# Performance work log

Measured on AMD Instinct MI355X. Metric: run time of the kernel, lower is better.

## Reference

```python
import jax, jax.numpy as jnp
import numpy as np

B, S, E, H, EDGE = 2, 2048, 512, 8, 16
D = E // H  # head_dim = 64


def setup_inputs() -> dict:
    key = jax.random.key(0)
    ks = jax.random.split(key, 10)
    s = 0.02
    return {
        "q": jax.random.normal(ks[0], (B, S, E), dtype=jnp.float32),
        "k": jax.random.normal(ks[1], (B, S, E), dtype=jnp.float32),
        "v": jax.random.normal(ks[2], (B, S, E), dtype=jnp.float32),
        "p": jax.random.normal(ks[3], (B, S, S, EDGE), dtype=jnp.float32),
        "in_proj_w": jax.random.normal(ks[4], (3 * E, E), dtype=jnp.float32) * s,
        "in_proj_b": jnp.zeros((3 * E,), dtype=jnp.float32),
        "out_proj_w": jax.random.normal(ks[5], (E, E), dtype=jnp.float32) * s,
        "out_proj_b": jnp.zeros((E,), dtype=jnp.float32),
        "edge_w": jax.random.normal(ks[6], (H, EDGE), dtype=jnp.float32) * s,
        "edge_b": jnp.zeros((H,), dtype=jnp.float32),
    }


def reference(q, k, v, p, in_proj_w, in_proj_b, out_proj_w, out_proj_b, edge_w, edge_b):
    b, s, e = q.shape
    # edge features -> per-head additive bias: [b,sq,sk,edge] -> [b,h,sq,sk]
    bias = jnp.einsum("bqke,he->bhqk", p, edge_w) + edge_b[None, :, None, None]

    # packed qkv projections (torch Linear: y = x W^T + b)
    wq, wk, wv = jnp.split(in_proj_w, 3, axis=0)
    bq, bk, bv = jnp.split(in_proj_b, 3, axis=0)
    qh = (q @ wq.T + bq).reshape(b, s, H, D).transpose(0, 2, 1, 3)  # bhqd
    kh = (k @ wk.T + bk).reshape(b, s, H, D).transpose(0, 2, 1, 3)  # bhkd
    vh = (v @ wv.T + bv).reshape(b, s, H, D).transpose(0, 2, 1, 3)  # bhkd

    scale = 1.0 / jnp.sqrt(jnp.float32(D))
    scores = jnp.einsum("bhqd,bhkd->bhqk", qh, kh) * scale + bias
    attn = jax.nn.softmax(scores, axis=-1)
    ctx = jnp.einsum("bhqk,bhkd->bhqd", attn, vh)  # [b,h,s,d]
    ctx = ctx.transpose(0, 2, 1, 3).reshape(b, s, e)
    return ctx @ out_proj_w.T + out_proj_b
```

## Files before the change

kernel.cpp:

```cpp
#include <hip/hip_runtime.h>

#define NB 2
#define NS 2048
#define NE 512
#define NH 8
#define ND 64
#define NEDGE 16

typedef unsigned short u16;
typedef __attribute__((ext_vector_type(4))) float f32x4;
typedef __attribute__((ext_vector_type(8))) short bf16x8;

__device__ __forceinline__ u16 f2bf(float f) {
  unsigned u = __float_as_uint(f);
  u += 0x7FFFu + ((u >> 16) & 1u);
  return (u16)(u >> 16);
}
__device__ __forceinline__ float bf2f(u16 h) {
  return __uint_as_float(((unsigned)h) << 16);
}
__device__ __forceinline__ void gload16(const void* g, void* l) {
  __builtin_amdgcn_global_load_lds(
      (const __attribute__((address_space(1))) unsigned*)g,
      (__attribute__((address_space(3))) unsigned*)l, 16, 0, 0);
}

__global__ void k_cvt(const float* __restrict__ in, u16* __restrict__ out, int n4) {
  int i = blockIdx.x * 256 + threadIdx.x;
  if (i >= n4) return;
  float4 v = ((const float4*)in)[i];
  ushort4 o;
  o.x = f2bf(v.x); o.y = f2bf(v.y); o.z = f2bf(v.z); o.w = f2bf(v.w);
  ((ushort4*)out)[i] = o;
}

__device__ __forceinline__ void gemm128_core(const u16* __restrict__ A,
                                             const u16* __restrict__ W,
                                             u16* As, u16* Bs,
                                             int mt, f32x4 acc[4][4]) {
  const int tid = threadIdx.x, wave = tid >> 6, lane = tid & 63;
  const int g = lane >> 4, c = lane & 15;
  const int wm = wave >> 1, wn = wave & 1;
  for (int kt = 0; kt < 16; ++kt) {
#pragma unroll
    for (int r = 0; r < 2; ++r) {
      int seg = wave + 4 * r;
      int idx = seg * 64 + lane;
      int row = idx >> 2, colB = idx & 3;
      gload16(A + (size_t)(mt * 128 + row) * 512 + kt * 32 + colB * 8,
              (char*)As + seg * 1024);
      gload16(W + (size_t)row * 512 + kt * 32 + colB * 8,
              (char*)Bs + seg * 1024);
    }
    __syncthreads();
    bf16x8 af[4], bw[4];
#pragma unroll
    for (int mb = 0; mb < 4; ++mb)
      af[mb] = *(const bf16x8*)&As[(wm * 64 + mb * 16 + c) * 32 + 8 * g];
#pragma unroll
    for (int nb = 0; nb < 4; ++nb)
      bw[nb] = *(const bf16x8*)&Bs[(wn * 64 + nb * 16 + c) * 32 + 8 * g];
#pragma unroll
    for (int mb = 0; mb < 4; ++mb)
#pragma unroll
      for (int nb = 0; nb < 4; ++nb)
        acc[mb][nb] = __builtin_amdgcn_mfma_f32_16x16x32_bf16(
            af[mb], bw[nb], acc[mb][nb], 0, 0, 0);
    __syncthreads();
  }
}

__launch_bounds__(256)
__global__ void k_proj(const u16* __restrict__ qbf, const u16* __restrict__ kbf,
                       const u16* __restrict__ vbf, const u16* __restrict__ wbf,
                       const float* __restrict__ bin,
                       u16* __restrict__ qh, u16* __restrict__ kh,
                       u16* __restrict__ vt) {
  __shared__ __align__(16) u16 As[4096];
  __shared__ __align__(16) u16 Bs[4096];
  const int tid = threadIdx.x, wave = tid >> 6, lane = tid & 63;
  const int g = lane >> 4, c = lane & 15;
  const int wm = wave >> 1, wn = wave & 1;
  const int mt = blockIdx.x;
  const int chunk = blockIdx.y >> 2, ntl = blockIdx.y & 3;
  const u16* A = chunk == 0 ? qbf : (chunk == 1 ? kbf : vbf);
  const u16* W = wbf + (size_t)(chunk * 512 + ntl * 128) * 512;

  f32x4 acc[4][4];
#pragma unroll
  for (int i = 0; i < 4; ++i)
#pragma unroll
    for (int j = 0; j < 4; ++j) acc[i][j] = (f32x4){0.f, 0.f, 0.f, 0.f};

  gemm128_core(A, W, As, Bs, mt, acc);

#pragma unroll
  for (int mb = 0; mb < 4; ++mb) {
#pragma unroll
    for (int nb = 0; nb < 4; ++nb) {
      int ncl = ntl * 128 + wn * 64 + nb * 16 + c;
      float bv = bin[chunk * 512 + ncl];
      int h = ncl >> 6, d = ncl & 63;
      int m0 = mt * 128 + wm * 64 + mb * 16 + g * 4;
      int b = m0 >> 11, s0 = m0 & 2047;
      if (chunk == 2) {
        ushort4 o;
        o.x = f2bf(acc[mb][nb][0] + bv);
        o.y = f2bf(acc[mb][nb][1] + bv);
        o.z = f2bf(acc[mb][nb][2] + bv);
        o.w = f2bf(acc[mb][nb][3] + bv);
        *(ushort4*)&vt[((size_t)(b * 8 + h) * 64 + d) * 2048 + s0] = o;
      } else {
        u16* dst = (chunk == 0) ? qh : kh;
        float sc = (chunk == 0) ? 0.125f : 1.0f;
#pragma unroll
        for (int r = 0; r < 4; ++r)
          dst[((size_t)(b * 8 + h) * 2048 + s0 + r) * 64 + d] =
              f2bf((acc[mb][nb][r] + bv) * sc);
      }
    }
  }
}

__launch_bounds__(256)
__global__ void k_bias(const float* __restrict__ p, const float* __restrict__ ewg,
                       const float* __restrict__ ebg, u16* __restrict__ bias,
                       int q0, int QC) {
  __shared__ float ew[NH * NEDGE];
  __shared__ float eb[NH];
  int tid = threadIdx.x;
  if (tid < NH * NEDGE) ew[tid] = ewg[tid];
  if (tid < NH) eb[tid] = ebg[tid];
  __syncthreads();
  int pi = blockIdx.x * 256 + tid;
  int total = NB * QC * NS;
  if (pi >= total) return;
  int k = pi & (NS - 1);
  int t2 = pi >> 11;
  int b = (t2 >= QC) ? 1 : 0;
  int ql = t2 - b * QC;
  int q = q0 + ql;

  const float* pv = p + (((size_t)(b * NS + q) * NS) + k) * NEDGE;
  float4 v0 = ((const float4*)pv)[0];
  float4 v1 = ((const float4*)pv)[1];
  float4 v2 = ((const float4*)pv)[2];
  float4 v3 = ((const float4*)pv)[3];
  float x[16] = {v0.x, v0.y, v0.z, v0.w, v1.x, v1.y, v1.z, v1.w,
                 v2.x, v2.y, v2.z, v2.w, v3.x, v3.y, v3.z, v3.w};
  float acc[NH];
#pragma unroll
  for (int h = 0; h < NH; ++h) {
    float a = eb[h];
#pragma unroll
    for (int e = 0; e < NEDGE; ++e) a += x[e] * ew[h * NEDGE + e];
    acc[h] = a;
  }
#pragma unroll
  for (int h = 0; h < NH; ++h)
    bias[((size_t)(b * 8 + h) * QC + ql) * NS + k] = f2bf(acc[h]);
}

__device__ __forceinline__ float redmax16(float x) {
  x = fmaxf(x, __shfl_xor(x, 1));
  x = fmaxf(x, __shfl_xor(x, 2));
  x = fmaxf(x, __shfl_xor(x, 4));
  x = fmaxf(x, __shfl_xor(x, 8));
  return x;
}
__device__ __forceinline__ float redsum16(float x) {
  x += __shfl_xor(x, 1); x += __shfl_xor(x, 2);
  x += __shfl_xor(x, 4); x += __shfl_xor(x, 8);
  return x;
}

__launch_bounds__(256)
__global__ void k_attn(const u16* __restrict__ qh, const u16* __restrict__ kh,
                       const u16* __restrict__ vt, const u16* __restrict__ biasb,
                       u16* __restrict__ ctx, int q0, int QC) {
  __shared__ __align__(16) u16 P_s[4 * 16 * 64];
  const int tid = threadIdx.x, wave = tid >> 6, lane = tid & 63;
  const int g = lane >> 4, c = lane & 15;
  const int qt = blockIdx.x, h = blockIdx.y, b = blockIdx.z;
  const int bh = b * 8 + h;
  const int q_chunk = qt * 64 + wave * 16;
  const int q_glob = q0 + q_chunk;
  u16* Pw = P_s + wave * 1024;

  const u16* Qb = qh + ((size_t)bh * 2048 + q_glob + c) * 64;
  bf16x8 qf0 = *(const bf16x8*)(Qb + 8 * g);
  bf16x8 qf1 = *(const bf16x8*)(Qb + 32 + 8 * g);

  const u16* Kb = kh + (size_t)bh * 2048 * 64;
  const u16* Vb = vt + (size_t)bh * 64 * 2048;
  const u16* Bb = biasb + (size_t)bh * QC * 2048;

  f32x4 o[4];
#pragma unroll
  for (int i = 0; i < 4; ++i) o[i] = (f32x4){0.f, 0.f, 0.f, 0.f};
  float mrow[4] = {-1e30f, -1e30f, -1e30f, -1e30f};
  float lrow[4] = {0.f, 0.f, 0.f, 0.f};

  for (int kt = 0; kt < 2048; kt += 64) {
    f32x4 sc[4];
#pragma unroll
    for (int nb = 0; nb < 4; ++nb) {
      const u16* kp = Kb + (size_t)(kt + nb * 16 + c) * 64 + 8 * g;
      bf16x8 b0 = *(const bf16x8*)kp;
      bf16x8 b1 = *(const bf16x8*)(kp + 32);
      f32x4 z = (f32x4){0.f, 0.f, 0.f, 0.f};
      z = __builtin_amdgcn_mfma_f32_16x16x32_bf16(qf0, b0, z, 0, 0, 0);
      z = __builtin_amdgcn_mfma_f32_16x16x32_bf16(qf1, b1, z, 0, 0, 0);
      sc[nb] = z;
    }
#pragma unroll
    for (int nb = 0; nb < 4; ++nb) {
#pragma unroll
      for (int r = 0; r < 4; ++r) {
        int ql_ = q_chunk + g * 4 + r;
        sc[nb][r] += bf2f(Bb[(size_t)ql_ * 2048 + kt + nb * 16 + c]);
      }
    }
    float mnew[4], scl[4];
#pragma unroll
    for (int r = 0; r < 4; ++r) {
      float mx = fmaxf(fmaxf(sc[0][r], sc[1][r]), fmaxf(sc[2][r], sc[3][r]));
      mx = redmax16(mx);
      mnew[r] = fmaxf(mrow[r], mx);
      scl[r] = __expf(mrow[r] - mnew[r]);
      mrow[r] = mnew[r];
    }
    float rsum[4] = {0.f, 0.f, 0.f, 0.f};
#pragma unroll
    for (int nb = 0; nb < 4; ++nb)
#pragma unroll
      for (int r = 0; r < 4; ++r) {
        float e = __expf(sc[nb][r] - mnew[r]);
        sc[nb][r] = e;
        rsum[r] += e;
      }
#pragma unroll
    for (int r = 0; r < 4; ++r) {
      float s = redsum16(rsum[r]);
      lrow[r] = lrow[r] * scl[r] + s;
    }
#pragma unroll
    for (int nd = 0; nd < 4; ++nd)
#pragma unroll
      for (int r = 0; r < 4; ++r) o[nd][r] *= scl[r];

#pragma unroll
    for (int nb = 0; nb < 4; ++nb)
#pragma unroll
      for (int r = 0; r < 4; ++r) {
        int rr = g * 4 + r, kk = nb * 16 + c;
        Pw[rr * 64 + (kk ^ ((rr & 7) << 3))] = f2bf(sc[nb][r]);
      }
    bf16x8 pa0, pa1;
    {
      int rr = c;
      pa0 = *(const bf16x8*)&Pw[rr * 64 + ((8 * g) ^ ((rr & 7) << 3))];
      pa1 = *(const bf16x8*)&Pw[rr * 64 + ((32 + 8 * g) ^ ((rr & 7) << 3))];
    }
#pragma unroll
    for (int nd = 0; nd < 4; ++nd) {
      const u16* vp = Vb + (size_t)(nd * 16 + c) * 2048 + kt;
      bf16x8 v0 = *(const bf16x8*)(vp + 8 * g);
      bf16x8 v1 = *(const bf16x8*)(vp + 32 + 8 * g);
      o[nd] = __builtin_amdgcn_mfma_f32_16x16x32_bf16(pa0, v0, o[nd], 0, 0, 0);
      o[nd] = __builtin_amdgcn_mfma_f32_16x16x32_bf16(pa1, v1, o[nd], 0, 0, 0);
    }
  }
  float inv[4];
#pragma unroll
  for (int r = 0; r < 4; ++r) inv[r] = 1.0f / lrow[r];
#pragma unroll
  for (int nd = 0; nd < 4; ++nd)
#pragma unroll
    for (int r = 0; r < 4; ++r) {
      int s_glob = q_glob + g * 4 + r;
      ctx[(size_t)(b * 2048 + s_glob) * 512 + h * 64 + nd * 16 + c] =
          f2bf(o[nd][r] * inv[r]);
    }
}

__launch_bounds__(256)
__global__ void k_outproj(const u16* __restrict__ ctx, const u16* __restrict__ wobf,
                          const float* __restrict__ bout, float* __restrict__ out) {
  __shared__ __align__(16) u16 As[4096];
  __shared__ __align__(16) u16 Bs[4096];
  const int tid = threadIdx.x, wave = tid >> 6, lane = tid & 63;
  const int g = lane >> 4, c = lane & 15;
  const int wm = wave >> 1, wn = wave & 1;
  const int mt = blockIdx.x, nt = blockIdx.y;
  const u16* W = wobf + (size_t)(nt * 128) * 512;

  f32x4 acc[4][4];
#pragma unroll
  for (int i = 0; i < 4; ++i)
#pragma unroll
    for (int j = 0; j < 4; ++j) acc[i][j] = (f32x4){0.f, 0.f, 0.f, 0.f};

  gemm128_core(ctx, W, As, Bs, mt, acc);

#pragma unroll
  for (int mb = 0; mb < 4; ++mb)
#pragma unroll
    for (int nb = 0; nb < 4; ++nb) {
      int n = nt * 128 + wn * 64 + nb * 16 + c;
      float bv = bout[n];
      int m0 = mt * 128 + wm * 64 + mb * 16 + g * 4;
#pragma unroll
      for (int r = 0; r < 4; ++r)
        out[(size_t)(m0 + r) * 512 + n] = acc[mb][nb][r] + bv;
    }
}

extern "C" void kernel_launch(void* const* d_in, const int* in_sizes, int n_in,
                              void* d_out, int out_size, void* d_ws, size_t ws_size,
                              hipStream_t stream) {
  (void)in_sizes; (void)n_in; (void)out_size;
  const float* q     = (const float*)d_in[0];
  const float* k     = (const float*)d_in[1];
  const float* v     = (const float*)d_in[2];
  const float* p     = (const float*)d_in[3];
  const float* w_in  = (const float*)d_in[4];
  const float* b_in  = (const float*)d_in[5];
  const float* w_out = (const float*)d_in[6];
  const float* b_out = (const float*)d_in[7];
  const float* ew    = (const float*)d_in[8];
  const float* eb    = (const float*)d_in[9];
  float* out = (float*)d_out;

  char* ws = (char*)d_ws;
  size_t off = 0;
  auto alloc = [&](size_t bytes) {
    void* r = ws + off;
    off += (bytes + 255) & ~(size_t)255;
    return r;
  };
  const size_t NTOK = (size_t)NB * NS;
  u16* qbf  = (u16*)alloc(NTOK * NE * 2);
  u16* kbf  = (u16*)alloc(NTOK * NE * 2);
  u16* vbf  = (u16*)alloc(NTOK * NE * 2);
  u16* wbf  = (u16*)alloc((size_t)3 * NE * NE * 2);
  u16* wobf = (u16*)alloc((size_t)NE * NE * 2);
  u16* qhb  = (u16*)alloc(NTOK * NE * 2);
  u16* khb  = (u16*)alloc(NTOK * NE * 2);
  u16* vtb  = (u16*)alloc(NTOK * NE * 2);
  u16* ctxb = (u16*)alloc(NTOK * NE * 2);

  size_t rem = (ws_size > off) ? (ws_size - off) : 0;
  int QC = 2048;
  while (QC > 64 && (size_t)NB * NH * QC * NS * 2 > rem) QC >>= 1;
  u16* biasb = (u16*)alloc((size_t)NB * NH * QC * NS * 2);

  int n4;
  n4 = (int)(NTOK * NE / 4);
  k_cvt<<<n4 / 256, 256, 0, stream>>>(q, qbf, n4);
  k_cvt<<<n4 / 256, 256, 0, stream>>>(k, kbf, n4);
  k_cvt<<<n4 / 256, 256, 0, stream>>>(v, vbf, n4);
  n4 = 3 * NE * NE / 4;
  k_cvt<<<n4 / 256, 256, 0, stream>>>(w_in, wbf, n4);
  n4 = NE * NE / 4;
  k_cvt<<<n4 / 256, 256, 0, stream>>>(w_out, wobf, n4);

  k_proj<<<dim3(32, 12), 256, 0, stream>>>(qbf, kbf, vbf, wbf, b_in, qhb, khb, vtb);

  for (int q0 = 0; q0 < NS; q0 += QC) {
    int pairs = NB * QC * NS;
    k_bias<<<pairs / 256, 256, 0, stream>>>(p, ew, eb, biasb, q0, QC);
    k_attn<<<dim3(QC / 64, NH, NB), 256, 0, stream>>>(qhb, khb, vtb, biasb, ctxb, q0, QC);
  }

  k_outproj<<<dim3(32, 4), 256, 0, stream>>>(ctxb, wobf, b_out, out);
}
```

Before: 904.5 us.

## Fuse edge-bias projection into attention kernel with double-buffered LDS staging of p

Removes the separate bias kernel and the bf16 bias buffer. Each block now handles 16 query rows for all 8 heads, one head per wave. It streams the p tile into shared memory once through double-buffered global_load_lds, with swizzled offsets, and computes the per-head bias inside the attention loop. The aim is to read the large p tensor once and skip writing and re-reading the materialized bias. In exchange each block uses 128KB+ of shared memory, which limits occupancy. The block-to-work mapping is also tuned to XCDs.

```diff
diff --git a/kernel.cpp b/kernel.cpp
--- a/kernel.cpp
+++ b/kernel.cpp
@@ -15,9 +15,6 @@
   unsigned u = __float_as_uint(f);
   u += 0x7FFFu + ((u >> 16) & 1u);
   return (u16)(u >> 16);
-}
-__device__ __forceinline__ float bf2f(u16 h) {
-  return __uint_as_float(((unsigned)h) << 16);
 }
 __device__ __forceinline__ void gload16(const void* g, void* l) {
   __builtin_amdgcn_global_load_lds(
@@ -122,45 +119,6 @@
   }
 }
 
-__launch_bounds__(256)
-__global__ void k_bias(const float* __restrict__ p, const float* __restrict__ ewg,
-                       const float* __restrict__ ebg, u16* __restrict__ bias,
-                       int q0, int QC) {
-  __shared__ float ew[NH * NEDGE];
-  __shared__ float eb[NH];
-  int tid = threadIdx.x;
-  if (tid < NH * NEDGE) ew[tid] = ewg[tid];
-  if (tid < NH) eb[tid] = ebg[tid];
-  __syncthreads();
-  int pi = blockIdx.x * 256 + tid;
-  int total = NB * QC * NS;
-  if (pi >= total) return;
-  int k = pi & (NS - 1);
-  int t2 = pi >> 11;
-  int b = (t2 >= QC) ? 1 : 0;
-  int ql = t2 - b * QC;
-  int q = q0 + ql;
-
-  const float* pv = p + (((size_t)(b * NS + q) * NS) + k) * NEDGE;
-  float4 v0 = ((const float4*)pv)[0];
-  float4 v1 = ((const float4*)pv)[1];
-  float4 v2 = ((const float4*)pv)[2];
-  float4 v3 = ((const float4*)pv)[3];
-  float x[16] = {v0.x, v0.y, v0.z, v0.w, v1.x, v1.y, v1.z, v1.w,
-                 v2.x, v2.y, v2.z, v2.w, v3.x, v3.y, v3.z, v3.w};
-  float acc[NH];
-#pragma unroll
-  for (int h = 0; h < NH; ++h) {
-    float a = eb[h];
-#pragma unroll
-    for (int e = 0; e < NEDGE; ++e) a += x[e] * ew[h * NEDGE + e];
-    acc[h] = a;
-  }
-#pragma unroll
-  for (int h = 0; h < NH; ++h)
-    bias[((size_t)(b * 8 + h) * QC + ql) * NS + k] = f2bf(acc[h]);
-}
-
 __device__ __forceinline__ float redmax16(float x) {
   x = fmaxf(x, __shfl_xor(x, 1));
   x = fmaxf(x, __shfl_xor(x, 2));
@@ -174,26 +132,47 @@
   return x;
 }
 
-__launch_bounds__(256)
-__global__ void k_attn(const u16* __restrict__ qh, const u16* __restrict__ kh,
-                       const u16* __restrict__ vt, const u16* __restrict__ biasb,
-                       u16* __restrict__ ctx, int q0, int QC) {
-  __shared__ __align__(16) u16 P_s[4 * 16 * 64];
-  const int tid = threadIdx.x, wave = tid >> 6, lane = tid & 63;
+__launch_bounds__(512, 2)
+__global__ void k_fattn(const float* __restrict__ p,
+                        const float* __restrict__ ewg, const float* __restrict__ ebg,
+                        const u16* __restrict__ qh, const u16* __restrict__ kh,
+                        const u16* __restrict__ vt, u16* __restrict__ ctx) {
+  __shared__ __align__(16) float p_s[2][16384];
+  __shared__ __align__(16) u16 P_s[8][1024];
+  const int tid = threadIdx.x;
+  const int wave = tid >> 6, lane = tid & 63;
   const int g = lane >> 4, c = lane & 15;
-  const int qt = blockIdx.x, h = blockIdx.y, b = blockIdx.z;
+  const int h = wave;
+  const int bid = blockIdx.x;
+  const int xcd = bid & 7, idx = bid >> 3;
+  const int b = xcd >> 2;
+  const int qt = (xcd & 3) * 32 + idx;
+  const int q0 = qt * 16;
   const int bh = b * 8 + h;
-  const int q_chunk = qt * 64 + wave * 16;
-  const int q_glob = q0 + q_chunk;
-  u16* Pw = P_s + wave * 1024;
-
-  const u16* Qb = qh + ((size_t)bh * 2048 + q_glob + c) * 64;
+  const int sl = (c >> 1) & 3;
+  u16* Pw = P_s[wave];
+
+  float ewh[16];
+#pragma unroll
+  for (int e = 0; e < 16; ++e) ewh[e] = ewg[h * 16 + e];
+  const float ebh = ebg[h];
+
+  const u16* Qb = qh + ((size_t)bh * 2048 + q0 + c) * 64;
   bf16x8 qf0 = *(const bf16x8*)(Qb + 8 * g);
   bf16x8 qf1 = *(const bf16x8*)(Qb + 32 + 8 * g);
-
   const u16* Kb = kh + (size_t)bh * 2048 * 64;
   const u16* Vb = vt + (size_t)bh * 64 * 2048;
-  const u16* Bb = biasb + (size_t)bh * QC * 2048;
+
+  const float* pb = p + (size_t)(b * 2048 + q0) * 2048 * 16;
+  int soff[8], doff[8];
+#pragma unroll
+  for (int i = 0; i < 8; ++i) {
+    int u = i * 512 + tid;
+    int ecp = u & 3, kk = (u >> 2) & 63, qq = u >> 8;
+    int ecl = ecp ^ ((kk >> 1) & 3);
+    soff[i] = (qq * 2048 + kk) * 16 + ecl * 4;
+    doff[i] = u * 16;
+  }
 
   f32x4 o[4];
 #pragma unroll
@@ -201,7 +180,44 @@
   float mrow[4] = {-1e30f, -1e30f, -1e30f, -1e30f};
   float lrow[4] = {0.f, 0.f, 0.f, 0.f};
 
-  for (int kt = 0; kt < 2048; kt += 64) {
+#pragma unroll
+  for (int i = 0; i < 8; ++i)
+    gload16(pb + soff[i], (char*)p_s + doff[i]);
+
+  for (int t = 0; t < 32; ++t) {
+    const int kt = t * 64;
+    asm volatile("s_waitcnt vmcnt(0)" ::: "memory");
+    __builtin_amdgcn_s_barrier();
+    __builtin_amdgcn_sched_barrier(0);
+    if (t < 31) {
+      const float* src = pb + (size_t)(kt + 64) * 16;
+      char* dst = (char*)p_s + ((t + 1) & 1) * 65536;
+#pragma unroll
+      for (int i = 0; i < 8; ++i)
+        gload16(src + soff[i], dst + doff[i]);
+    }
+    __builtin_amdgcn_sched_barrier(0);
+    const float* pc = p_s[t & 1];
+
+    float bv[4][4];
+#pragma unroll
+    for (int nb = 0; nb < 4; ++nb) {
+#pragma unroll
+      for (int r = 0; r < 4; ++r) {
+        const float* ps = pc + (g * 4 + r) * 1024 + (nb * 16 + c) * 16;
+        f32x4 a0 = *(const f32x4*)(ps + (0 ^ sl) * 4);
+        f32x4 a1 = *(const f32x4*)(ps + (1 ^ sl) * 4);
+        f32x4 a2 = *(const f32x4*)(ps + (2 ^ sl) * 4);
+        f32x4 a3 = *(const f32x4*)(ps + (3 ^ sl) * 4);
+        float d = ebh;
+        d += a0[0]*ewh[0] + a0[1]*ewh[1] + a0[2]*ewh[2] + a0[3]*ewh[3];
+        d += a1[0]*ewh[4] + a1[1]*ewh[5] + a1[2]*ewh[6] + a1[3]*ewh[7];
+        d += a2[0]*ewh[8] + a2[1]*ewh[9] + a2[2]*ewh[10] + a2[3]*ewh[11];
+        d += a3[0]*ewh[12] + a3[1]*ewh[13] + a3[2]*ewh[14] + a3[3]*ewh[15];
+        bv[nb][r] = d;
+      }
+    }
+
     f32x4 sc[4];
 #pragma unroll
     for (int nb = 0; nb < 4; ++nb) {
@@ -214,13 +230,10 @@
       sc[nb] = z;
     }
 #pragma unroll
-    for (int nb = 0; nb < 4; ++nb) {
-#pragma unroll
-      for (int r = 0; r < 4; ++r) {
-        int ql_ = q_chunk + g * 4 + r;
-        sc[nb][r] += bf2f(Bb[(size_t)ql_ * 2048 + kt + nb * 16 + c]);
-      }
-    }
+    for (int nb = 0; nb < 4; ++nb)
+#pragma unroll
+      for (int r = 0; r < 4; ++r) sc[nb][r] += bv[nb][r];
+
     float mnew[4], scl[4];
 #pragma unroll
     for (int r = 0; r < 4; ++r) {
@@ -271,6 +284,7 @@
       o[nd] = __builtin_amdgcn_mfma_f32_16x16x32_bf16(pa1, v1, o[nd], 0, 0, 0);
     }
   }
+
   float inv[4];
 #pragma unroll
   for (int r = 0; r < 4; ++r) inv[r] = 1.0f / lrow[r];
@@ -278,7 +292,7 @@
   for (int nd = 0; nd < 4; ++nd)
 #pragma unroll
     for (int r = 0; r < 4; ++r) {
-      int s_glob = q_glob + g * 4 + r;
+      int s_glob = q0 + g * 4 + r;
       ctx[(size_t)(b * 2048 + s_glob) * 512 + h * 64 + nd * 16 + c] =
           f2bf(o[nd][r] * inv[r]);
     }
@@ -319,7 +333,7 @@
 extern "C" void kernel_launch(void* const* d_in, const int* in_sizes, int n_in,
                               void* d_out, int out_size, void* d_ws, size_t ws_size,
                               hipStream_t stream) {
-  (void)in_sizes; (void)n_in; (void)out_size;
+  (void)in_sizes; (void)n_in; (void)out_size; (void)ws_size;
   const float* q     = (const float*)d_in[0];
   const float* k     = (const float*)d_in[1];
   const float* v     = (const float*)d_in[2];
@@ -350,11 +364,6 @@
   u16* vtb  = (u16*)alloc(NTOK * NE * 2);
   u16* ctxb = (u16*)alloc(NTOK * NE * 2);
 
-  size_t rem = (ws_size > off) ? (ws_size - off) : 0;
-  int QC = 2048;
-  while (QC > 64 && (size_t)NB * NH * QC * NS * 2 > rem) QC >>= 1;
-  u16* biasb = (u16*)alloc((size_t)NB * NH * QC * NS * 2);
-
   int n4;
   n4 = (int)(NTOK * NE / 4);
   k_cvt<<<n4 / 256, 256, 0, stream>>>(q, qbf, n4);
@@ -367,11 +376,7 @@
 
   k_proj<<<dim3(32, 12), 256, 0, stream>>>(qbf, kbf, vbf, wbf, b_in, qhb, khb, vtb);
 
-  for (int q0 = 0; q0 < NS; q0 += QC) {
-    int pairs = NB * QC * NS;
-    k_bias<<<pairs / 256, 256, 0, stream>>>(p, ew, eb, biasb, q0, QC);
-    k_attn<<<dim3(QC / 64, NH, NB), 256, 0, stream>>>(qhb, khb, vtb, biasb, ctxb, q0, QC);
-  }
+  k_fattn<<<256, 512, 0, stream>>>(p, ew, eb, qhb, khb, vtb, ctxb);
 
   k_outproj<<<dim3(32, 4), 256, 0, stream>>>(ctxb, wobf, b_out, out);
 }
```

After: 894.1 us. About the same (-1.2%).
